# Kernel optimization log

Measured on AMD Instinct MI355X. Metric: run time of the kernel, lower is better.

## Reference

```python
import jax, jax.numpy as jnp
import numpy as np

N, E = 50000, 800000
IN, HID, H, OUT = 128, 32, 4, 32
NEG_SLOPE = 0.2


def _gatv2_layer(x, edge_index, Wl, bl, Wr, br, att, bias, heads, ch, concat):
    """One GATv2Conv layer (PyG semantics: add self-loops, lin_l on source,
    lin_r on target, e = att . leaky_relu(gl_src + gr_dst), segment softmax
    over incoming edges of each target, scatter-add weighted source messages)."""
    n = x.shape[0]
    loop = jnp.arange(n)
    src = jnp.concatenate([edge_index[0], loop])
    dst = jnp.concatenate([edge_index[1], loop])

    gl = (x @ Wl + bl).reshape(n, heads, ch)   # source transform [N,H,C]
    gr = (x @ Wr + br).reshape(n, heads, ch)   # target transform [N,H,C]

    m = jax.nn.leaky_relu(gl[src] + gr[dst], NEG_SLOPE)   # [E+N,H,C]
    e = jnp.einsum('ehc,hc->eh', m, att)                   # [E+N,H]

    # numerically stable segment softmax over dst
    emax = jax.lax.stop_gradient(jax.ops.segment_max(e, dst, num_segments=n))
    ex = jnp.exp(e - emax[dst])
    denom = jax.ops.segment_sum(ex, dst, num_segments=n)
    alpha = ex / denom[dst]                                # [E+N,H]

    out = jax.ops.segment_sum(alpha[:, :, None] * gl[src], dst, num_segments=n)  # [N,H,C]
    out = out.reshape(n, heads * ch) if concat else out.mean(axis=1)
    return out + bias


def setup_inputs() -> dict:
    key = jax.random.key(0)
    ks = jax.random.split(key, 16)
    s = 0.05
    return {
        'x': jax.random.normal(ks[0], (N, IN), dtype=jnp.float32),
        'edge_index': jax.random.randint(ks[1], (2, E), 0, N, dtype=jnp.int32),
        # layer 1: IN -> HID, H heads, concat
        'Wl1': jax.random.normal(ks[2], (IN, H * HID), dtype=jnp.float32) * s,
        'bl1': jnp.zeros((H * HID,), dtype=jnp.float32),
        'Wr1': jax.random.normal(ks[3], (IN, H * HID), dtype=jnp.float32) * s,
        'br1': jnp.zeros((H * HID,), dtype=jnp.float32),
        'att1': jax.random.normal(ks[4], (H, HID), dtype=jnp.float32) * s,
        'bias1': jnp.zeros((H * HID,), dtype=jnp.float32),
        # layer 2: H*HID -> OUT, 1 head, no concat
        'Wl2': jax.random.normal(ks[5], (H * HID, OUT), dtype=jnp.float32) * s,
        'bl2': jnp.zeros((OUT,), dtype=jnp.float32),
        'Wr2': jax.random.normal(ks[6], (H * HID, OUT), dtype=jnp.float32) * s,
        'br2': jnp.zeros((OUT,), dtype=jnp.float32),
        'att2': jax.random.normal(ks[7], (1, OUT), dtype=jnp.float32) * s,
        'bias2': jnp.zeros((OUT,), dtype=jnp.float32),
    }


def reference(x, edge_index, Wl1, bl1, Wr1, br1, att1, bias1,
              Wl2, bl2, Wr2, br2, att2, bias2):
    h = jax.nn.elu(_gatv2_layer(x, edge_index, Wl1, bl1, Wr1, br1, att1, bias1, H, HID, True))
    # dropout inactive in eval mode
    return _gatv2_layer(h, edge_index, Wl2, bl2, Wr2, br2, att2, bias2, 1, OUT, False)
```

## Files before the change

### kernel.cpp

```cpp
#include <hip/hip_runtime.h>

#define NNODES 50000
#define NEDGES 800000
#define ETOT   (NNODES + NEDGES)
#define NEG 0.2f
#define BKTS 196
#define P1E 4096
#define NP1 ((ETOT + P1E - 1) / P1E)

typedef unsigned short ushort_t;
typedef unsigned int uint_t;
typedef __attribute__((ext_vector_type(8))) short short8;
typedef __attribute__((ext_vector_type(4))) float f32x4;

__device__ __forceinline__ ushort_t f2bf(float f) {
  uint_t u = __float_as_uint(f);
  u += 0x7FFFu + ((u >> 16) & 1u);
  return (ushort_t)(u >> 16);
}
__device__ __forceinline__ float bf2f(ushort_t h) {
  return __uint_as_float((uint_t)h << 16);
}

__global__ __launch_bounds__(256) void coarse_hist(const int* __restrict__ ei,
                                                   int* __restrict__ pcnt) {
  __shared__ int c[BKTS];
  for (int i = threadIdx.x; i < BKTS; i += 256) c[i] = 0;
  __syncthreads();
  int e0 = blockIdx.x * P1E;
#pragma unroll
  for (int t = 0; t < P1E / 256; ++t) {
    int i = e0 + t * 256 + (int)threadIdx.x;
    if (i < ETOT) {
      int dst = (i < NEDGES) ? ei[NEDGES + i] : (i - NEDGES);
      atomicAdd(&c[dst >> 8], 1);
    }
  }
  __syncthreads();
  for (int i = threadIdx.x; i < BKTS; i += 256)
    pcnt[i * NP1 + blockIdx.x] = c[i];
}

__global__ __launch_bounds__(64) void coarse_scan(const int* __restrict__ pcnt,
                                                  int* __restrict__ goffArr,
                                                  int* __restrict__ tot) {
  int b = blockIdx.x;
  int lane = threadIdx.x;
  int carry = 0;
  for (int k0 = 0; k0 < NP1; k0 += 64) {
    int k = k0 + lane;
    int v = (k < NP1) ? pcnt[b * NP1 + k] : 0;
    int s = v;
    for (int off = 1; off < 64; off <<= 1) {
      int u = __shfl_up(s, off);
      if (lane >= off) s += u;
    }
    if (k < NP1) goffArr[b * NP1 + k] = carry + s - v;
    carry += __shfl(s, 63);
  }
  if (lane == 0) tot[b] = carry;
}

__global__ __launch_bounds__(64) void bucket_scan(const int* __restrict__ tot,
                                                  int* __restrict__ bucketStart,
                                                  int* __restrict__ rowptr) {
  int lane = threadIdx.x;
  int carry = 0;
  for (int k0 = 0; k0 < BKTS; k0 += 64) {
    int k = k0 + lane;
    int v = (k < BKTS) ? tot[k] : 0;
    int s = v;
    for (int off = 1; off < 64; off <<= 1) {
      int u = __shfl_up(s, off);
      if (lane >= off) s += u;
    }
    if (k < BKTS) bucketStart[k] = carry + s - v;
    carry += __shfl(s, 63);
  }
  if (lane == 0) {
    bucketStart[BKTS] = carry;
    rowptr[NNODES] = ETOT;
  }
}

__global__ __launch_bounds__(256) void bin_phase1(const int* __restrict__ ei,
                                                  const int* __restrict__ bucketStart,
                                                  const int* __restrict__ goffArr,
                                                  uint_t* __restrict__ binned) {
  __shared__ int cnt[BKTS], pref[BKTS], fillL[BKTS];
  __shared__ uint_t stage[P1E];
  int e0 = blockIdx.x * P1E;
  for (int i = threadIdx.x; i < BKTS; i += 256) { cnt[i] = 0; fillL[i] = 0; }
  __syncthreads();
  uint_t mypk[P1E / 256];
  int mybkt[P1E / 256];
#pragma unroll
  for (int t = 0; t < P1E / 256; ++t) {
    int i = e0 + t * 256 + (int)threadIdx.x;
    if (i < ETOT) {
      int dst = (i < NEDGES) ? ei[NEDGES + i] : (i - NEDGES);
      int src = (i < NEDGES) ? ei[i] : dst;
      int b = dst >> 8;
      mypk[t] = (uint_t)src | ((uint_t)(dst & 255) << 16) | ((uint_t)b << 24);
      mybkt[t] = b;
      atomicAdd(&cnt[b], 1);
    } else mybkt[t] = -1;
  }
  __syncthreads();
  if (threadIdx.x == 0) {
    int r = 0;
    for (int b = 0; b < BKTS; ++b) { pref[b] = r; r += cnt[b]; }
  }
  __syncthreads();
#pragma unroll
  for (int t = 0; t < P1E / 256; ++t) {
    if (mybkt[t] >= 0) {
      int p = pref[mybkt[t]] + atomicAdd(&fillL[mybkt[t]], 1);
      stage[p] = mypk[t];
    }
  }
  __syncthreads();
  int total = (e0 + P1E <= ETOT) ? P1E : (ETOT - e0);
  for (int j = threadIdx.x; j < total; j += 256) {
    uint_t pk = stage[j];
    int b = pk >> 24;
    binned[bucketStart[b] + goffArr[b * NP1 + blockIdx.x] + (j - pref[b])] = pk;
  }
}

__global__ __launch_bounds__(256) void bin_phase2(const uint_t* __restrict__ binned,
                                                  const int* __restrict__ bucketStart,
                                                  int* __restrict__ rowptr,
                                                  int* __restrict__ csrc) {
  __shared__ int cnt[256], pref[256], fillL[256];
  __shared__ int outS[8192];
  int b = blockIdx.x;
  int base = bucketStart[b];
  int cntAll = bucketStart[b + 1] - base;
  cnt[threadIdx.x] = 0; fillL[threadIdx.x] = 0;
  __syncthreads();
  for (int j = threadIdx.x; j < cntAll; j += 256)
    atomicAdd(&cnt[(binned[base + j] >> 16) & 255], 1);
  __syncthreads();
  if (threadIdx.x == 0) {
    int r = 0;
    for (int i = 0; i < 256; ++i) { pref[i] = r; r += cnt[i]; }
  }
  __syncthreads();
  int node = b * 256 + (int)threadIdx.x;
  if (node < NNODES) rowptr[node] = base + pref[threadIdx.x];
  for (int j = threadIdx.x; j < cntAll; j += 256) {
    uint_t pk = binned[base + j];
    int d = (pk >> 16) & 255;
    int p = pref[d] + atomicAdd(&fillL[d], 1);
    outS[p] = (int)(pk & 0xFFFF);
  }
  __syncthreads();
  for (int j = threadIdx.x; j < cntAll; j += 256)
    csrc[base + j] = outS[j];
}

__global__ __launch_bounds__(256) void prep_w(const float* __restrict__ Wl1,
                                              const float* __restrict__ Wr1,
                                              ushort_t* __restrict__ WtHi,
                                              ushort_t* __restrict__ WtLo) {
  int k = blockIdx.x;
  int n = threadIdx.x;
  float w = (n < 128) ? Wl1[k * 128 + n] : Wr1[k * 128 + (n - 128)];
  ushort_t h = f2bf(w);
  WtHi[n * 128 + k] = h;
  WtLo[n * 128 + k] = f2bf(w - bf2f(h));
}

__global__ __launch_bounds__(256) void gemm1_mfma(
    const float* __restrict__ x,
    const ushort_t* __restrict__ WtHi, const ushort_t* __restrict__ WtLo,
    const float* __restrict__ bl1, const float* __restrict__ br1,
    const float* __restrict__ att,
    ushort_t* __restrict__ gl1, ushort_t* __restrict__ gr1,
    float* __restrict__ elt, float* __restrict__ ern) {
  constexpr int LDA = 132;
  __shared__ __align__(16) char smem[32 * 260 * 4];
  ushort_t (*Ahi)[LDA] = (ushort_t(*)[LDA])smem;
  ushort_t (*Alo)[LDA] = (ushort_t(*)[LDA])(smem + 32 * LDA * 2);
  float (*Cs)[260] = (float(*)[260])smem;
  int m0 = blockIdx.x * 32;
  int tid = threadIdx.x;
#pragma unroll
  for (int i = 0; i < 4; ++i) {
    int it = i * 256 + tid;
    int row = it >> 5, c4 = it & 31;
    int gm = m0 + row;
    float4 v = (gm < NNODES) ? *(const float4*)&x[(size_t)gm * 128 + 4 * c4]
                             : make_float4(0.f, 0.f, 0.f, 0.f);
    ushort_t h0 = f2bf(v.x), h1 = f2bf(v.y), h2 = f2bf(v.z), h3 = f2bf(v.w);
    ushort_t l0 = f2bf(v.x - bf2f(h0)), l1 = f2bf(v.y - bf2f(h1));
    ushort_t l2 = f2bf(v.z - bf2f(h2)), l3 = f2bf(v.w - bf2f(h3));
    uint2 ph, pl;
    ph.x = (uint_t)h0 | ((uint_t)h1 << 16); ph.y = (uint_t)h2 | ((uint_t)h3 << 16);
    pl.x = (uint_t)l0 | ((uint_t)l1 << 16); pl.y = (uint_t)l2 | ((uint_t)l3 << 16);
    *(uint2*)&Ahi[row][4 * c4] = ph;
    *(uint2*)&Alo[row][4 * c4] = pl;
  }
  __syncthreads();
  int wave = tid >> 6, lane = tid & 63;
  int quad = lane >> 4, nl = lane & 15;
  int nb = wave * 64;
  f32x4 acc[2][4];
#pragma unroll
  for (int tm = 0; tm < 2; ++tm)
#pragma unroll
    for (int tn = 0; tn < 4; ++tn) acc[tm][tn] = (f32x4){0.f, 0.f, 0.f, 0.f};

#pragma unroll
  for (int kc = 0; kc < 4; ++kc) {
    int klane = kc * 32 + quad * 8;
    short8 ah[2], al[2], bh[4], bl[4];
#pragma unroll
    for (int tm = 0; tm < 2; ++tm) {
      ah[tm] = *(const short8*)&Ahi[16 * tm + nl][klane];
      al[tm] = *(const short8*)&Alo[16 * tm + nl][klane];
    }
#pragma unroll
    for (int tn = 0; tn < 4; ++tn) {
      size_t wo = (size_t)(nb + 16 * tn + nl) * 128 + klane;
      bh[tn] = *(const short8*)&WtHi[wo];
      bl[tn] = *(const short8*)&WtLo[wo];
    }
#pragma unroll
    for (int tm = 0; tm < 2; ++tm)
#pragma unroll
      for (int tn = 0; tn < 4; ++tn) {
        acc[tm][tn] = __builtin_amdgcn_mfma_f32_16x16x32_bf16(ah[tm], bh[tn], acc[tm][tn], 0, 0, 0);
        acc[tm][tn] = __builtin_amdgcn_mfma_f32_16x16x32_bf16(ah[tm], bl[tn], acc[tm][tn], 0, 0, 0);
        acc[tm][tn] = __builtin_amdgcn_mfma_f32_16x16x32_bf16(al[tm], bh[tn], acc[tm][tn], 0, 0, 0);
      }
  }
  float bb[4];
#pragma unroll
  for (int tn = 0; tn < 4; ++tn) {
    int n = nb + 16 * tn + nl;
    bb[tn] = (n < 128) ? bl1[n] : br1[n - 128];
  }
  __syncthreads();
#pragma unroll
  for (int tm = 0; tm < 2; ++tm)
#pragma unroll
    for (int tn = 0; tn < 4; ++tn)
#pragma unroll
      for (int r = 0; r < 4; ++r)
        Cs[16 * tm + 4 * quad + r][nb + 16 * tn + nl] = acc[tm][tn][r] + bb[tn];
  __syncthreads();
#pragma unroll
  for (int i = 0; i < 2; ++i) {
    int it = i * 256 + tid;
    int row = it >> 4, oc = (it & 15) * 8;
    int gm = m0 + row;
    if (gm < NNODES) {
      uint4 pk;
      pk.x = (uint_t)f2bf(Cs[row][oc + 0]) | ((uint_t)f2bf(Cs[row][oc + 1]) << 16);
      pk.y = (uint_t)f2bf(Cs[row][oc + 2]) | ((uint_t)f2bf(Cs[row][oc + 3]) << 16);
      pk.z = (uint_t)f2bf(Cs[row][oc + 4]) | ((uint_t)f2bf(Cs[row][oc + 5]) << 16);
      pk.w = (uint_t)f2bf(Cs[row][oc + 6]) | ((uint_t)f2bf(Cs[row][oc + 7]) << 16);
      *(uint4*)&gl1[(size_t)gm * 128 + oc] = pk;
    }
  }
#pragma unroll
  for (int i = 0; i < 2; ++i) {
    int it = i * 256 + tid;
    int row = it >> 4, oc = (it & 15) * 8;
    int gm = m0 + row;
    if (gm < NNODES) {
      uint4 pk;
      pk.x = (uint_t)f2bf(Cs[row][128 + oc + 0]) | ((uint_t)f2bf(Cs[row][128 + oc + 1]) << 16);
      pk.y = (uint_t)f2bf(Cs[row][128 + oc + 2]) | ((uint_t)f2bf(Cs[row][128 + oc + 3]) << 16);
      pk.z = (uint_t)f2bf(Cs[row][128 + oc + 4]) | ((uint_t)f2bf(Cs[row][128 + oc + 5]) << 16);
      pk.w = (uint_t)f2bf(Cs[row][128 + oc + 6]) | ((uint_t)f2bf(Cs[row][128 + oc + 7]) << 16);
      *(uint4*)&gr1[(size_t)gm * 128 + oc] = pk;
    }
  }
  {
    int row = tid >> 3, part = tid & 7;
    int gm = m0 + row;
    if (gm < NNODES) {
      int hh = part & 3;
      int cbase = ((part & 4) ? 128 : 0) + hh * 32;
      float accd = 0.f;
#pragma unroll
      for (int c = 0; c < 32; c += 4) {
        float4 cv = *(const float4*)&Cs[row][cbase + c];
        float4 av = *(const float4*)&att[hh * 32 + c];
        accd = fmaf(cv.x, av.x, accd);
        accd = fmaf(cv.y, av.y, accd);
        accd = fmaf(cv.z, av.z, accd);
        accd = fmaf(cv.w, av.w, accd);
      }
      accd *= 0.6f;
      if (part < 4) elt[gm * 4 + hh] = accd;
      else          ern[gm * 4 + hh] = accd;
    }
  }
}

__global__ __launch_bounds__(128) void gemm2_tile(
    const ushort_t* __restrict__ A,
    const float* __restrict__ W1, const float* __restrict__ b1,
    const float* __restrict__ W2, const float* __restrict__ b2,
    const float* __restrict__ att,
    ushort_t* __restrict__ G1, ushort_t* __restrict__ G2,
    float* __restrict__ el2, float* __restrict__ er2) {
  constexpr int K = 128, KC = 32, BM = 128, BN = 64, MCOLS = 32, NT = 128;
  constexpr int LDA = BM + 4;
  __shared__ float AsT[KC][LDA];
  __shared__ float Ws[KC][BN];
  int row0 = blockIdx.x * BM;
  int tid = threadIdx.x;
  int tx = tid % (BN / 8), ty = tid / (BN / 8);
  float acc[8][8];
#pragma unroll
  for (int i = 0; i < 8; ++i)
#pragma unroll
    for (int j = 0; j < 8; ++j) acc[i][j] = 0.f;

  for (int kc = 0; kc < K; kc += KC) {
#pragma unroll
    for (int item = tid; item < BM * (KC / 4); item += NT) {
      int r = item >> 3, f4 = item & 7;
      int grow = row0 + r;
      uint2 u = (grow < NNODES)
          ? *(const uint2*)&A[(size_t)grow * K + kc + 4 * f4]
          : make_uint2(0u, 0u);
      AsT[4 * f4 + 0][r] = __uint_as_float(u.x << 16);
      AsT[4 * f4 + 1][r] = __uint_as_float(u.x & 0xffff0000u);
      AsT[4 * f4 + 2][r] = __uint_as_float(u.y << 16);
      AsT[4 * f4 + 3][r] = __uint_as_float(u.y & 0xffff0000u);
    }
#pragma unroll
    for (int item = tid; item < KC * (BN / 4); item += NT) {
      int k = item / (BN / 4), c4 = item % (BN / 4);
      int ccat = 4 * c4;
      const float* src = (ccat < MCOLS)
          ? &W1[(size_t)(kc + k) * MCOLS + ccat]
          : &W2[(size_t)(kc + k) * MCOLS + ccat - MCOLS];
      *(float4*)&Ws[k][4 * c4] = *(const float4*)src;
    }
    __syncthreads();
#pragma unroll 8
    for (int k = 0; k < KC; ++k) {
      float4 a0 = *(const float4*)&AsT[k][4 * ty];
      float4 a1 = *(const float4*)&AsT[k][BM / 2 + 4 * ty];
      float4 w0 = *(const float4*)&Ws[k][4 * tx];
      float4 w1 = *(const float4*)&Ws[k][BN / 2 + 4 * tx];
      float av[8] = {a0.x, a0.y, a0.z, a0.w, a1.x, a1.y, a1.z, a1.w};
      float wv[8] = {w0.x, w0.y, w0.z, w0.w, w1.x, w1.y, w1.z, w1.w};
#pragma unroll
      for (int i = 0; i < 8; ++i)
#pragma unroll
        for (int j = 0; j < 8; ++j) acc[i][j] = fmaf(av[i], wv[j], acc[i][j]);
    }
    __syncthreads();
  }
  float4 a6 = *(const float4*)&att[4 * tx];
  a6.x *= 0.6f; a6.y *= 0.6f; a6.z *= 0.6f; a6.w *= 0.6f;
#pragma unroll
  for (int i = 0; i < 8; ++i) {
    int row = row0 + (i < 4 ? 4 * ty + i : BM / 2 + 4 * ty + (i - 4));
    if (row >= NNODES) continue;
    float pel = 0.f, per2 = 0.f;
#pragma unroll
    for (int jj = 0; jj < 2; ++jj) {
      int ccat = (jj == 0 ? 4 * tx : BN / 2 + 4 * tx);
      float o0 = acc[i][4 * jj + 0], o1 = acc[i][4 * jj + 1];
      float o2 = acc[i][4 * jj + 2], o3 = acc[i][4 * jj + 3];
      if (ccat < MCOLS) {
        float4 bb = *(const float4*)&b1[ccat];
        o0 += bb.x; o1 += bb.y; o2 += bb.z; o3 += bb.w;
        pel = fmaf(o0, a6.x, pel); pel = fmaf(o1, a6.y, pel);
        pel = fmaf(o2, a6.z, pel); pel = fmaf(o3, a6.w, pel);
        uint2 pk;
        pk.x = (uint_t)f2bf(o0) | ((uint_t)f2bf(o1) << 16);
        pk.y = (uint_t)f2bf(o2) | ((uint_t)f2bf(o3) << 16);
        *(uint2*)&G1[(size_t)row * MCOLS + ccat] = pk;
      } else {
        int c = ccat - MCOLS;
        float4 bb = *(const float4*)&b2[c];
        o0 += bb.x; o1 += bb.y; o2 += bb.z; o3 += bb.w;
        per2 = fmaf(o0, a6.x, per2); per2 = fmaf(o1, a6.y, per2);
        per2 = fmaf(o2, a6.z, per2); per2 = fmaf(o3, a6.w, per2);
        uint2 pk;
        pk.x = (uint_t)f2bf(o0) | ((uint_t)f2bf(o1) << 16);
        pk.y = (uint_t)f2bf(o2) | ((uint_t)f2bf(o3) << 16);
        *(uint2*)&G2[(size_t)row * MCOLS + c] = pk;
      }
    }
    pel  += __shfl_xor(pel, 1);  pel  += __shfl_xor(pel, 2);  pel  += __shfl_xor(pel, 4);
    per2 += __shfl_xor(per2, 1); per2 += __shfl_xor(per2, 2); per2 += __shfl_xor(per2, 4);
    if (tx == 0) { el2[row] = pel; er2[row] = per2; }
  }
}

__global__ __launch_bounds__(128) void gat1_edge(const int* __restrict__ rowptr,
                          const int* __restrict__ csrc,
                          const ushort_t* __restrict__ glb,
                          const ushort_t* __restrict__ grb,
                          const float* __restrict__ elt,
                          const float* __restrict__ ern,
                          const float* __restrict__ att, const float* __restrict__ bias,
                          ushort_t* __restrict__ hout) {
  int node = blockIdx.x * 2 + (threadIdx.x >> 6);
  if (node >= NNODES) return;
  int lane = threadIdx.x & 63;
  int eslot = lane >> 4;
  int q = lane & 15;
  int c8 = q * 8;
  int head = q >> 2;
  float4 a0 = *(const float4*)(att + c8);
  float4 a1 = *(const float4*)(att + c8 + 4);
  a0.x *= 0.4f; a0.y *= 0.4f; a0.z *= 0.4f; a0.w *= 0.4f;
  a1.x *= 0.4f; a1.y *= 0.4f; a1.z *= 0.4f; a1.w *= 0.4f;
  uint4 ug = *(const uint4*)(grb + (size_t)node * 128 + c8);
  float4 gr0, gr1v;
  gr0.x = __uint_as_float(ug.x << 16);  gr0.y = __uint_as_float(ug.x & 0xffff0000u);
  gr0.z = __uint_as_float(ug.y << 16);  gr0.w = __uint_as_float(ug.y & 0xffff0000u);
  gr1v.x = __uint_as_float(ug.z << 16); gr1v.y = __uint_as_float(ug.z & 0xffff0000u);
  gr1v.z = __uint_as_float(ug.w << 16); gr1v.w = __uint_as_float(ug.w & 0xffff0000u);
  float eb = ern[node * 4 + head];
  int start = rowptr[node], end = rowptr[node + 1];
  float denom = 0.f;
  float4 A0 = make_float4(0.f, 0.f, 0.f, 0.f);
  float4 A1 = make_float4(0.f, 0.f, 0.f, 0.f);
  const char* glc = (const char*)glb;
  const char* elc = (const char*)elt;
  uint_t coff = (uint_t)(c8 * 2);
  uint_t hoff = (uint_t)(head * 4);
  for (int b = start; b < end; b += 64) {
    int nb = end - b; if (nb > 64) nb = 64;
    int sidx = (lane < nb) ? csrc[b + lane] : 0;
    for (int j = 0; j < nb; j += 4) {
      int jj = j + eslot;
      bool pv = jj < nb;
      int s = __shfl(sidx, jj);
      float el_s = *(const float*)(elc + (((uint_t)s << 4) + hoff));
      uint4 up = *(const uint4*)(glc + (((uint_t)s << 8) + coff));
      float4 g0, g1;
      g0.x = __uint_as_float(up.x << 16);
      g0.y = __uint_as_float(up.x & 0xffff0000u);
      g0.z = __uint_as_float(up.y << 16);
      g0.w = __uint_as_float(up.y & 0xffff0000u);
      g1.x = __uint_as_float(up.z << 16);
      g1.y = __uint_as_float(up.z & 0xffff0000u);
      g1.z = __uint_as_float(up.w << 16);
      g1.w = __uint_as_float(up.w & 0xffff0000u);
      float t, v;
      t = g0.x + gr0.x;  v = a0.x * fabsf(t);
      t = g0.y + gr0.y;  v = fmaf(a0.y, fabsf(t), v);
      t = g0.z + gr0.z;  v = fmaf(a0.z, fabsf(t), v);
      t = g0.w + gr0.w;  v = fmaf(a0.w, fabsf(t), v);
      t = g1.x + gr1v.x; v = fmaf(a1.x, fabsf(t), v);
      t = g1.y + gr1v.y; v = fmaf(a1.y, fabsf(t), v);
      t = g1.z + gr1v.z; v = fmaf(a1.z, fabsf(t), v);
      t = g1.w + gr1v.w; v = fmaf(a1.w, fabsf(t), v);
      v += __shfl_xor(v, 1); v += __shfl_xor(v, 2);
      v += el_s + eb;
      float ex = pv ? __expf(v) : 0.f;
      denom += ex;
      A0.x = fmaf(ex, g0.x, A0.x); A0.y = fmaf(ex, g0.y, A0.y);
      A0.z = fmaf(ex, g0.z, A0.z); A0.w = fmaf(ex, g0.w, A0.w);
      A1.x = fmaf(ex, g1.x, A1.x); A1.y = fmaf(ex, g1.y, A1.y);
      A1.z = fmaf(ex, g1.z, A1.z); A1.w = fmaf(ex, g1.w, A1.w);
    }
  }
  denom += __shfl_xor(denom, 16); denom += __shfl_xor(denom, 32);
  A0.x += __shfl_xor(A0.x, 16); A0.x += __shfl_xor(A0.x, 32);
  A0.y += __shfl_xor(A0.y, 16); A0.y += __shfl_xor(A0.y, 32);
  A0.z += __shfl_xor(A0.z, 16); A0.z += __shfl_xor(A0.z, 32);
  A0.w += __shfl_xor(A0.w, 16); A0.w += __shfl_xor(A0.w, 32);
  A1.x += __shfl_xor(A1.x, 16); A1.x += __shfl_xor(A1.x, 32);
  A1.y += __shfl_xor(A1.y, 16); A1.y += __shfl_xor(A1.y, 32);
  A1.z += __shfl_xor(A1.z, 16); A1.z += __shfl_xor(A1.z, 32);
  A1.w += __shfl_xor(A1.w, 16); A1.w += __shfl_xor(A1.w, 32);
  float inv = __builtin_amdgcn_rcpf(denom);
  if (eslot == 0) {
    float4 bv = *(const float4*)(bias + c8);
    float o0 = A0.x * inv + bv.x, o1 = A0.y * inv + bv.y;
    float o2 = A0.z * inv + bv.z, o3 = A0.w * inv + bv.w;
    o0 = o0 > 0.f ? o0 : __expf(o0) - 1.f;
    o1 = o1 > 0.f ? o1 : __expf(o1) - 1.f;
    o2 = o2 > 0.f ? o2 : __expf(o2) - 1.f;
    o3 = o3 > 0.f ? o3 : __expf(o3) - 1.f;
    uint2 pk;
    pk.x = (uint_t)f2bf(o0) | ((uint_t)f2bf(o1) << 16);
    pk.y = (uint_t)f2bf(o2) | ((uint_t)f2bf(o3) << 16);
    *(uint2*)&hout[(size_t)node * 128 + c8] = pk;
  } else if (eslot == 1) {
    float4 bv = *(const float4*)(bias + c8 + 4);
    float o0 = A1.x * inv + bv.x, o1 = A1.y * inv + bv.y;
    float o2 = A1.z * inv + bv.z, o3 = A1.w * inv + bv.w;
    o0 = o0 > 0.f ? o0 : __expf(o0) - 1.f;
    o1 = o1 > 0.f ? o1 : __expf(o1) - 1.f;
    o2 = o2 > 0.f ? o2 : __expf(o2) - 1.f;
    o3 = o3 > 0.f ? o3 : __expf(o3) - 1.f;
    uint2 pk;
    pk.x = (uint_t)f2bf(o0) | ((uint_t)f2bf(o1) << 16);
    pk.y = (uint_t)f2bf(o2) | ((uint_t)f2bf(o3) << 16);
    *(uint2*)&hout[(size_t)node * 128 + c8 + 4] = pk;
  }
}

__global__ __launch_bounds__(128) void gat2_edge(const int* __restrict__ rowptr,
                          const int* __restrict__ csrc,
                          const ushort_t* __restrict__ gl, const ushort_t* __restrict__ gr,
                          const float* __restrict__ el2, const float* __restrict__ er2,
                          const float* __restrict__ att, const float* __restrict__ bias,
                          float* __restrict__ out) {
  int node = blockIdx.x * 2 + (threadIdx.x >> 6);
  if (node >= NNODES) return;
  int lane = threadIdx.x & 63;
  int eslot = lane >> 3;
  int q = lane & 7;
  int c4 = q * 4;
  float4 avc = *(const float4*)(att + c4);
  avc.x *= 0.4f; avc.y *= 0.4f; avc.z *= 0.4f; avc.w *= 0.4f;
  uint2 ugr = *(const uint2*)(gr + (size_t)node * 32 + c4);
  float4 grd;
  grd.x = __uint_as_float(ugr.x << 16); grd.y = __uint_as_float(ugr.x & 0xffff0000u);
  grd.z = __uint_as_float(ugr.y << 16); grd.w = __uint_as_float(ugr.y & 0xffff0000u);
  float eb = er2[node];
  int start = rowptr[node], end = rowptr[node + 1];
  float denom = 0.f;
  float4 A = make_float4(0.f, 0.f, 0.f, 0.f);
  const char* glc = (const char*)gl;
  uint_t coff = (uint_t)(c4 * 2);
  for (int b = start; b < end; b += 64) {
    int nb = end - b; if (nb > 64) nb = 64;
    int sidx = (lane < nb) ? csrc[b + lane] : 0;
    for (int j = 0; j < nb; j += 8) {
      int jj = j + eslot;
      bool pv = jj < nb;
      int s = __shfl(sidx, jj);
      float el_s = el2[s];
      uint2 ugl = *(const uint2*)(glc + (((uint_t)s << 6) + coff));
      float4 g;
      g.x = __uint_as_float(ugl.x << 16); g.y = __uint_as_float(ugl.x & 0xffff0000u);
      g.z = __uint_as_float(ugl.y << 16); g.w = __uint_as_float(ugl.y & 0xffff0000u);
      float t, v;
      t = g.x + grd.x; v = avc.x * fabsf(t);
      t = g.y + grd.y; v = fmaf(avc.y, fabsf(t), v);
      t = g.z + grd.z; v = fmaf(avc.z, fabsf(t), v);
      t = g.w + grd.w; v = fmaf(avc.w, fabsf(t), v);
      v += __shfl_xor(v, 1); v += __shfl_xor(v, 2); v += __shfl_xor(v, 4);
      v += el_s + eb;
      float ex = pv ? __expf(v) : 0.f;
      denom += ex;
      A.x = fmaf(ex, g.x, A.x); A.y = fmaf(ex, g.y, A.y);
      A.z = fmaf(ex, g.z, A.z); A.w = fmaf(ex, g.w, A.w);
    }
  }
  denom += __shfl_xor(denom, 8); denom += __shfl_xor(denom, 16); denom += __shfl_xor(denom, 32);
  A.x += __shfl_xor(A.x, 8); A.x += __shfl_xor(A.x, 16); A.x += __shfl_xor(A.x, 32);
  A.y += __shfl_xor(A.y, 8); A.y += __shfl_xor(A.y, 16); A.y += __shfl_xor(A.y, 32);
  A.z += __shfl_xor(A.z, 8); A.z += __shfl_xor(A.z, 16); A.z += __shfl_xor(A.z, 32);
  A.w += __shfl_xor(A.w, 8); A.w += __shfl_xor(A.w, 16); A.w += __shfl_xor(A.w, 32);
  if (eslot == 0) {
    float inv = __builtin_amdgcn_rcpf(denom);
    float4 bv = *(const float4*)(bias + c4);
    float4 o;
    o.x = A.x * inv + bv.x; o.y = A.y * inv + bv.y;
    o.z = A.z * inv + bv.z; o.w = A.w * inv + bv.w;
    *(float4*)(out + (size_t)node * 32 + c4) = o;
  }
}

extern "C" void kernel_launch(void* const* d_in, const int* in_sizes, int n_in,
                              void* d_out, int out_size, void* d_ws, size_t ws_size,
                              hipStream_t stream) {
  const float* x     = (const float*)d_in[0];
  const int*   ei    = (const int*)  d_in[1];
  const float* Wl1   = (const float*)d_in[2];
  const float* bl1   = (const float*)d_in[3];
  const float* Wr1   = (const float*)d_in[4];
  const float* br1   = (const float*)d_in[5];
  const float* att1  = (const float*)d_in[6];
  const float* bias1 = (const float*)d_in[7];
  const float* Wl2   = (const float*)d_in[8];
  const float* bl2   = (const float*)d_in[9];
  const float* Wr2   = (const float*)d_in[10];
  const float* br2   = (const float*)d_in[11];
  const float* att2  = (const float*)d_in[12];
  const float* bias2 = (const float*)d_in[13];
  float* out = (float*)d_out;

  char* w = (char*)d_ws;
  auto carve = [&](size_t bytes) {
    char* p = w;
    w += (bytes + 255) & ~(size_t)255;
    return p;
  };
  ushort_t* gl1 = (ushort_t*)carve((size_t)NNODES * 128 * 2);
  ushort_t* gr1 = (ushort_t*)carve((size_t)NNODES * 128 * 2);
  ushort_t* h   = (ushort_t*)carve((size_t)NNODES * 128 * 2);
  ushort_t* gl2 = (ushort_t*)carve((size_t)NNODES * 32 * 2);
  ushort_t* gr2 = (ushort_t*)carve((size_t)NNODES * 32 * 2);
  ushort_t* WtHi = (ushort_t*)carve((size_t)256 * 128 * 2);
  ushort_t* WtLo = (ushort_t*)carve((size_t)256 * 128 * 2);
  float* elt = (float*)carve((size_t)NNODES * 4 * 4);
  float* ern = (float*)carve((size_t)NNODES * 4 * 4);
  float* el2 = (float*)carve((size_t)NNODES * 4);
  float* er2 = (float*)carve((size_t)NNODES * 4);
  int* pcnt    = (int*)carve((size_t)NP1 * BKTS * 4);
  int* goffArr = (int*)carve((size_t)NP1 * BKTS * 4);
  int* tot     = (int*)carve((size_t)BKTS * 4);
  int* bucketStart = (int*)carve((size_t)(BKTS + 1) * 4);
  int* rowptr = (int*)carve((size_t)(NNODES + 1) * 4);
  uint_t* binned = (uint_t*)carve((size_t)ETOT * 4);
  int* csrc = (int*)carve((size_t)ETOT * 4);

  prep_w<<<128, 256, 0, stream>>>(Wl1, Wr1, WtHi, WtLo);
  coarse_hist<<<NP1, 256, 0, stream>>>(ei, pcnt);
  coarse_scan<<<BKTS, 64, 0, stream>>>(pcnt, goffArr, tot);
  bucket_scan<<<1, 64, 0, stream>>>(tot, bucketStart, rowptr);
  bin_phase1<<<NP1, 256, 0, stream>>>(ei, bucketStart, goffArr, binned);
  bin_phase2<<<BKTS, 256, 0, stream>>>(binned, bucketStart, rowptr, csrc);

  gemm1_mfma<<<(NNODES + 31) / 32, 256, 0, stream>>>(x, WtHi, WtLo, bl1, br1, att1,
                                                     gl1, gr1, elt, ern);
  gat1_edge<<<(NNODES + 1) / 2, 128, 0, stream>>>(rowptr, csrc, gl1, gr1, elt, ern,
                                                  att1, bias1, h);
  gemm2_tile<<<(NNODES + 127) / 128, 128, 0, stream>>>(h, Wl2, bl2, Wr2, br2, att2,
                                                       gl2, gr2, el2, er2);
  gat2_edge<<<(NNODES + 1) / 2, 128, 0, stream>>>(rowptr, csrc, gl2, gr2, el2, er2,
                                                  att2, bias2, out);
}
```

Baseline: 271.8 us.

## Interleave per-head attention logits into padded gl1 rows and prefetch edge gathers

The source-side attention term elt is now stored inside each gl1 row, which is padded to 272 bytes, so one gather brings both features and logits. This removes a separate scattered load per edge. The edge loops in both GAT layers also software-prefetch the next edge's row before the current edge is processed, to hide gather latency. gemm1 writes its output tile to shared memory in two halves so the buffer shrinks, at the cost of an extra barrier pair. Padded rows are not a multiple of 256 bytes, which may split rows across cache lines.

After: 275.9 us. Within noise of the previous version (+1.5%).

```diff
diff --git a/kernel.cpp b/kernel.cpp
--- a/kernel.cpp
+++ b/kernel.cpp
@@ -178,12 +178,12 @@
     const float* __restrict__ bl1, const float* __restrict__ br1,
     const float* __restrict__ att,
     ushort_t* __restrict__ gl1, ushort_t* __restrict__ gr1,
-    float* __restrict__ elt, float* __restrict__ ern) {
+    float* __restrict__ ern) {
   constexpr int LDA = 132;
-  __shared__ __align__(16) char smem[32 * 260 * 4];
+  __shared__ __align__(16) char smem[32 * 132 * 4];
   ushort_t (*Ahi)[LDA] = (ushort_t(*)[LDA])smem;
   ushort_t (*Alo)[LDA] = (ushort_t(*)[LDA])(smem + 32 * LDA * 2);
-  float (*Cs)[260] = (float(*)[260])smem;
+  float (*Cs)[132] = (float(*)[132])smem;
   int m0 = blockIdx.x * 32;
   int tid = threadIdx.x;
 #pragma unroll
@@ -243,13 +243,15 @@
     bb[tn] = (n < 128) ? bl1[n] : br1[n - 128];
   }
   __syncthreads();
-#pragma unroll
-  for (int tm = 0; tm < 2; ++tm)
-#pragma unroll
-    for (int tn = 0; tn < 4; ++tn)
-#pragma unroll
-      for (int r = 0; r < 4; ++r)
-        Cs[16 * tm + 4 * quad + r][nb + 16 * tn + nl] = acc[tm][tn][r] + bb[tn];
+  if (wave < 2) {
+#pragma unroll
+    for (int tm = 0; tm < 2; ++tm)
+#pragma unroll
+      for (int tn = 0; tn < 4; ++tn)
+#pragma unroll
+        for (int r = 0; r < 4; ++r)
+          Cs[16 * tm + 4 * quad + r][nb + 16 * tn + nl] = acc[tm][tn][r] + bb[tn];
+  }
   __syncthreads();
 #pragma unroll
   for (int i = 0; i < 2; ++i) {
@@ -262,9 +264,37 @@
       pk.y = (uint_t)f2bf(Cs[row][oc + 2]) | ((uint_t)f2bf(Cs[row][oc + 3]) << 16);
       pk.z = (uint_t)f2bf(Cs[row][oc + 4]) | ((uint_t)f2bf(Cs[row][oc + 5]) << 16);
       pk.w = (uint_t)f2bf(Cs[row][oc + 6]) | ((uint_t)f2bf(Cs[row][oc + 7]) << 16);
-      *(uint4*)&gl1[(size_t)gm * 128 + oc] = pk;
-    }
-  }
+      *(uint4*)&gl1[(size_t)gm * 136 + oc] = pk;
+    }
+  }
+  {
+    int row = tid >> 3, part = tid & 7;
+    int gm = m0 + row;
+    if (part < 4 && gm < NNODES) {
+      float accd = 0.f;
+#pragma unroll
+      for (int c = 0; c < 32; c += 4) {
+        float4 cv = *(const float4*)&Cs[row][part * 32 + c];
+        float4 av = *(const float4*)&att[part * 32 + c];
+        accd = fmaf(cv.x, av.x, accd);
+        accd = fmaf(cv.y, av.y, accd);
+        accd = fmaf(cv.z, av.z, accd);
+        accd = fmaf(cv.w, av.w, accd);
+      }
+      *(float*)((char*)gl1 + (size_t)gm * 272 + 256 + part * 4) = 0.6f * accd;
+    }
+  }
+  __syncthreads();
+  if (wave >= 2) {
+#pragma unroll
+    for (int tm = 0; tm < 2; ++tm)
+#pragma unroll
+      for (int tn = 0; tn < 4; ++tn)
+#pragma unroll
+        for (int r = 0; r < 4; ++r)
+          Cs[16 * tm + 4 * quad + r][(nb - 128) + 16 * tn + nl] = acc[tm][tn][r] + bb[tn];
+  }
+  __syncthreads();
 #pragma unroll
   for (int i = 0; i < 2; ++i) {
     int it = i * 256 + tid;
@@ -272,32 +302,28 @@
     int gm = m0 + row;
     if (gm < NNODES) {
       uint4 pk;
-      pk.x = (uint_t)f2bf(Cs[row][128 + oc + 0]) | ((uint_t)f2bf(Cs[row][128 + oc + 1]) << 16);
-      pk.y = (uint_t)f2bf(Cs[row][128 + oc + 2]) | ((uint_t)f2bf(Cs[row][128 + oc + 3]) << 16);
-      pk.z = (uint_t)f2bf(Cs[row][128 + oc + 4]) | ((uint_t)f2bf(Cs[row][128 + oc + 5]) << 16);
-      pk.w = (uint_t)f2bf(Cs[row][128 + oc + 6]) | ((uint_t)f2bf(Cs[row][128 + oc + 7]) << 16);
+      pk.x = (uint_t)f2bf(Cs[row][oc + 0]) | ((uint_t)f2bf(Cs[row][oc + 1]) << 16);
+      pk.y = (uint_t)f2bf(Cs[row][oc + 2]) | ((uint_t)f2bf(Cs[row][oc + 3]) << 16);
+      pk.z = (uint_t)f2bf(Cs[row][oc + 4]) | ((uint_t)f2bf(Cs[row][oc + 5]) << 16);
+      pk.w = (uint_t)f2bf(Cs[row][oc + 6]) | ((uint_t)f2bf(Cs[row][oc + 7]) << 16);
       *(uint4*)&gr1[(size_t)gm * 128 + oc] = pk;
     }
   }
   {
     int row = tid >> 3, part = tid & 7;
     int gm = m0 + row;
-    if (gm < NNODES) {
-      int hh = part & 3;
-      int cbase = ((part & 4) ? 128 : 0) + hh * 32;
+    if (part < 4 && gm < NNODES) {
       float accd = 0.f;
 #pragma unroll
       for (int c = 0; c < 32; c += 4) {
-        float4 cv = *(const float4*)&Cs[row][cbase + c];
-        float4 av = *(const float4*)&att[hh * 32 + c];
+        float4 cv = *(const float4*)&Cs[row][part * 32 + c];
+        float4 av = *(const float4*)&att[part * 32 + c];
         accd = fmaf(cv.x, av.x, accd);
         accd = fmaf(cv.y, av.y, accd);
         accd = fmaf(cv.z, av.z, accd);
         accd = fmaf(cv.w, av.w, accd);
       }
-      accd *= 0.6f;
-      if (part < 4) elt[gm * 4 + hh] = accd;
-      else          ern[gm * 4 + hh] = accd;
+      ern[gm * 4 + part] = 0.6f * accd;
     }
   }
 }
@@ -403,7 +429,6 @@
                           const int* __restrict__ csrc,
                           const ushort_t* __restrict__ glb,
                           const ushort_t* __restrict__ grb,
-                          const float* __restrict__ elt,
                           const float* __restrict__ ern,
                           const float* __restrict__ att, const float* __restrict__ bias,
                           ushort_t* __restrict__ hout) {
@@ -430,18 +455,23 @@
   float4 A0 = make_float4(0.f, 0.f, 0.f, 0.f);
   float4 A1 = make_float4(0.f, 0.f, 0.f, 0.f);
   const char* glc = (const char*)glb;
-  const char* elc = (const char*)elt;
   uint_t coff = (uint_t)(c8 * 2);
-  uint_t hoff = (uint_t)(head * 4);
+  uint_t eloff = 256u + (uint_t)(head * 4);
   for (int b = start; b < end; b += 64) {
     int nb = end - b; if (nb > 64) nb = 64;
     int sidx = (lane < nb) ? csrc[b + lane] : 0;
+    int s0 = __shfl(sidx, eslot);
+    const char* rp = glc + (uint_t)s0 * 272u;
+    uint4 up = *(const uint4*)(rp + coff);
+    float el_s = *(const float*)(rp + eloff);
     for (int j = 0; j < nb; j += 4) {
-      int jj = j + eslot;
-      bool pv = jj < nb;
-      int s = __shfl(sidx, jj);
-      float el_s = *(const float*)(elc + (((uint_t)s << 4) + hoff));
-      uint4 up = *(const uint4*)(glc + (((uint_t)s << 8) + coff));
+      bool pv = (j + eslot) < nb;
+      int jn = j + 4 + eslot;
+      int jc = (jn < nb) ? jn : 0;
+      int sn = __shfl(sidx, jc);
+      const char* rpn = glc + (uint_t)sn * 272u;
+      uint4 upn = *(const uint4*)(rpn + coff);
+      float eln = *(const float*)(rpn + eloff);
       float4 g0, g1;
       g0.x = __uint_as_float(up.x << 16);
       g0.y = __uint_as_float(up.x & 0xffff0000u);
@@ -468,6 +498,7 @@
       A0.z = fmaf(ex, g0.z, A0.z); A0.w = fmaf(ex, g0.w, A0.w);
       A1.x = fmaf(ex, g1.x, A1.x); A1.y = fmaf(ex, g1.y, A1.y);
       A1.z = fmaf(ex, g1.z, A1.z); A1.w = fmaf(ex, g1.w, A1.w);
+      up = upn; el_s = eln;
     }
   }
   denom += __shfl_xor(denom, 16); denom += __shfl_xor(denom, 32);
@@ -534,12 +565,16 @@
   for (int b = start; b < end; b += 64) {
     int nb = end - b; if (nb > 64) nb = 64;
     int sidx = (lane < nb) ? csrc[b + lane] : 0;
+    int s0 = __shfl(sidx, eslot);
+    uint2 ugl = *(const uint2*)(glc + (((uint_t)s0 << 6) + coff));
+    float el_s = el2[s0];
     for (int j = 0; j < nb; j += 8) {
-      int jj = j + eslot;
-      bool pv = jj < nb;
-      int s = __shfl(sidx, jj);
-      float el_s = el2[s];
-      uint2 ugl = *(const uint2*)(glc + (((uint_t)s << 6) + coff));
+      bool pv = (j + eslot) < nb;
+      int jn = j + 8 + eslot;
+      int jc = (jn < nb) ? jn : 0;
+      int sn = __shfl(sidx, jc);
+      uint2 ugn = *(const uint2*)(glc + (((uint_t)sn << 6) + coff));
+      float eln = el2[sn];
       float4 g;
       g.x = __uint_as_float(ugl.x << 16); g.y = __uint_as_float(ugl.x & 0xffff0000u);
       g.z = __uint_as_float(ugl.y << 16); g.w = __uint_as_float(ugl.y & 0xffff0000u);
@@ -554,6 +589,7 @@
       denom += ex;
       A.x = fmaf(ex, g.x, A.x); A.y = fmaf(ex, g.y, A.y);
       A.z = fmaf(ex, g.z, A.z); A.w = fmaf(ex, g.w, A.w);
+      ugl = ugn; el_s = eln;
     }
   }
   denom += __shfl_xor(denom, 8); denom += __shfl_xor(denom, 16); denom += __shfl_xor(denom, 32);
@@ -596,14 +632,13 @@
     w += (bytes + 255) & ~(size_t)255;
     return p;
   };
-  ushort_t* gl1 = (ushort_t*)carve((size_t)NNODES * 128 * 2);
+  ushort_t* gl1 = (ushort_t*)carve((size_t)NNODES * 136 * 2);
   ushort_t* gr1 = (ushort_t*)carve((size_t)NNODES * 128 * 2);
   ushort_t* h   = (ushort_t*)carve((size_t)NNODES * 128 * 2);
   ushort_t* gl2 = (ushort_t*)carve((size_t)NNODES * 32 * 2);
   ushort_t* gr2 = (ushort_t*)carve((size_t)NNODES * 32 * 2);
   ushort_t* WtHi = (ushort_t*)carve((size_t)256 * 128 * 2);
   ushort_t* WtLo = (ushort_t*)carve((size_t)256 * 128 * 2);
-  float* elt = (float*)carve((size_t)NNODES * 4 * 4);
   float* ern = (float*)carve((size_t)NNODES * 4 * 4);
   float* el2 = (float*)carve((size_t)NNODES * 4);
   float* er2 = (float*)carve((size_t)NNODES * 4);
@@ -623,8 +658,8 @@
   bin_phase2<<<BKTS, 256, 0, stream>>>(binned, bucketStart, rowptr, csrc);
 
   gemm1_mfma<<<(NNODES + 31) / 32, 256, 0, stream>>>(x, WtHi, WtLo, bl1, br1, att1,
-                                                     gl1, gr1, elt, ern);
-  gat1_edge<<<(NNODES + 1) / 2, 128, 0, stream>>>(rowptr, csrc, gl1, gr1, elt, ern,
+                                                     gl1, gr1, ern);
+  gat1_edge<<<(NNODES + 1) / 2, 128, 0, stream>>>(rowptr, csrc, gl1, gr1, ern,
                                                   att1, bias1, h);
   gemm2_tile<<<(NNODES + 127) / 128, 128, 0, stream>>>(h, Wl2, bl2, Wr2, br2, att2,
                                                        gl2, gr2, el2, er2);
```
